# Optimization experiments

Measured on AMD Instinct MI355X. Metric: run time of the kernel, lower is better.

## Reference

```python
import jax, jax.numpy as jnp
import numpy as np

DIM_MSA = 256
DIM_PAIR = 128
DIM_HID = 32
EPS = 0.001
LN_EPS = 1e-5


def setup_inputs() -> dict:
    key = jax.random.key(0)
    ks = jax.random.split(key, 8)
    b, m, n = 1, 256, 384
    x = jax.random.normal(ks[0], (b, m, n, DIM_MSA), dtype=jnp.float32)
    mask = jax.random.randint(ks[1], (b, m, n), 0, 2).astype(jnp.int32)
    ln_g = jnp.ones((DIM_MSA,), jnp.float32)
    ln_b = jnp.zeros((DIM_MSA,), jnp.float32)
    s = 1.0 / np.sqrt(DIM_MSA)
    wl = jax.random.normal(ks[2], (DIM_MSA, DIM_HID), jnp.float32) * s
    bl = jnp.zeros((DIM_HID,), jnp.float32)
    wr = jax.random.normal(ks[3], (DIM_MSA, DIM_HID), jnp.float32) * s
    br = jnp.zeros((DIM_HID,), jnp.float32)
    wo = jax.random.normal(ks[4], (DIM_HID * DIM_HID, DIM_PAIR), jnp.float32) / np.sqrt(DIM_HID * DIM_HID)
    bo = jnp.zeros((DIM_PAIR,), jnp.float32)
    return {"x": x, "mask": mask, "ln_g": ln_g, "ln_b": ln_b,
            "wl": wl, "bl": bl, "wr": wr, "br": br, "wo": wo, "bo": bo}


def reference(x, mask, ln_g, ln_b, wl, bl, wr, br, wo, bo):
    # LayerNorm over last dim
    mu = jnp.mean(x, axis=-1, keepdims=True)
    var = jnp.mean(jnp.square(x - mu), axis=-1, keepdims=True)
    xn = (x - mu) * jax.lax.rsqrt(var + LN_EPS) * ln_g + ln_b
    left = xn @ wl + bl    # [b,m,n,c]
    right = xn @ wr + br   # [b,m,n,d]
    m = mask.astype(x.dtype)  # 0/1 mask [b,m,n]
    left = left * m[..., None]
    right = right * m[..., None]
    # masked outer-product sum over MSA dim m, no 6D materialization
    outer = jnp.einsum('bmic,bmjd->bijcd', left, right)
    b_, i_, j_ = outer.shape[0], outer.shape[1], outer.shape[2]
    outer = outer.reshape(b_, i_, j_, DIM_HID * DIM_HID)
    out = outer @ wo + bo  # [b,i,j,pairwise]
    cnt = jnp.einsum('bmi,bmj->bij', m, m)  # valid-pair counts
    return out / (cnt[..., None] + EPS)
```

## Files before the change

kernel.cpp:

```cpp
#include <hip/hip_runtime.h>
#include <hip/hip_bf16.h>
#include <stdint.h>


typedef float f32x4 __attribute__((ext_vector_type(4)));
typedef __bf16 bf16x8 __attribute__((ext_vector_type(8)));

#define NSEQ 384
#define NMSA 256

typedef const __attribute__((address_space(1))) unsigned int* gptr_t;
typedef __attribute__((address_space(3))) unsigned int* lptr_t;

__device__ __forceinline__ void gload_lds16(const void* g, void* l) {
    __builtin_amdgcn_global_load_lds((gptr_t)g, (lptr_t)l, 16, 0, 0);
}

__global__ __launch_bounds__(256) void prep_all_kernel(
    const float* __restrict__ wo,
    const float* __restrict__ wl, const float* __restrict__ wr,
    const float* __restrict__ bl, const float* __restrict__ br,
    const float* __restrict__ ln_g, const float* __restrict__ ln_b,
    const int* __restrict__ mask,
    __bf16* __restrict__ woT, __bf16* __restrict__ wg,
    float* __restrict__ Gc, float* __restrict__ B2,
    float* __restrict__ inv_cnt)
{
    const int blk = blockIdx.x;
    __shared__ int mi[NMSA];
    __shared__ float sg[4], sb[4];

    if (blk < 512) {
        int gid = blk * 256 + threadIdx.x;
        int p = gid >> 10, k = gid & 1023;
        woT[gid] = (__bf16)wo[k * 128 + p];
    } else if (blk < 576) {
        const int c = blk - 512;
        const int k = threadIdx.x;
        float w = (c < 32) ? wl[k * 32 + c] : wr[k * 32 + (c - 32)];
        __bf16 wgb = (__bf16)(w * ln_g[k]);
        wg[c * 256 + k] = wgb;
        float gsum = (float)wgb;
        float bsum = w * ln_b[k];
        for (int off = 32; off; off >>= 1) {
            gsum += __shfl_down(gsum, off);
            bsum += __shfl_down(bsum, off);
        }
        int wid = k >> 6, lane = k & 63;
        if (lane == 0) { sg[wid] = gsum; sb[wid] = bsum; }
        __syncthreads();
        if (k == 0) {
            Gc[c] = sg[0] + sg[1] + sg[2] + sg[3];
            B2[c] = sb[0] + sb[1] + sb[2] + sb[3] + ((c < 32) ? bl[c] : br[c - 32]);
        }
    } else {
        const int i = blk - 576;
        const int t = threadIdx.x;
        mi[t] = mask[t * NSEQ + i];
        __syncthreads();
        for (int j = t; j < NSEQ; j += 256) {
            int acc = 0;
            for (int m = 0; m < NMSA; ++m)
                acc += mi[m] & mask[m * NSEQ + j];
            inv_cnt[i * NSEQ + j] = 1.0f / ((float)acc + 0.001f);
        }
    }
}

__global__ __launch_bounds__(256) void ln_proj_kernel(
    const float* __restrict__ x, const int* __restrict__ mask,
    const __bf16* __restrict__ wg, const float* __restrict__ Gc,
    const float* __restrict__ B2,
    __bf16* __restrict__ leftT, __bf16* __restrict__ rightT)
{
    const int n = blockIdx.x % NSEQ;
    const int mh = blockIdx.x / NSEQ;
    const int m0 = mh * 128;
    const int tid = threadIdx.x;
    __shared__ __bf16 xnT[128 * 40];
    __shared__ float muS[128], rsS[128], maskS[128], GcS[64], B2S[64];

    if (tid < 64) { GcS[tid] = Gc[tid]; B2S[tid] = B2[tid]; }
    if (tid < 128) maskS[tid] = (float)mask[(m0 + tid) * NSEQ + n];

    const int wid = tid >> 6, lane = tid & 63;
    const int lhi = lane >> 4, llo = lane & 15;
    const int wrq = wid >> 1, wcq = wid & 1;
    float ps[4] = {}, pq[4] = {};
    f32x4 acc[2][4] = {};

    for (int k0 = 0; k0 < 256; k0 += 32) {
        #pragma unroll
        for (int cc = 0; cc < 4; ++cc) {
            int ch = tid + cc * 256;
            int mR = ch >> 3, c4 = ch & 7;
            f32x4 v = *reinterpret_cast<const f32x4*>(x + ((size_t)(m0 + mR) * NSEQ + n) * 256 + k0 + c4 * 4);
            ps[cc] += v[0] + v[1] + v[2] + v[3];
            pq[cc] += v[0]*v[0] + v[1]*v[1] + v[2]*v[2] + v[3]*v[3];
            __bf16* dst = xnT + mR * 40 + c4 * 4;
            dst[0] = (__bf16)v[0]; dst[1] = (__bf16)v[1];
            dst[2] = (__bf16)v[2]; dst[3] = (__bf16)v[3];
        }
        __syncthreads();
        bf16x8 af[2], bfr[4];
        #pragma unroll
        for (int fr = 0; fr < 2; ++fr)
            af[fr] = *reinterpret_cast<const bf16x8*>(wg + (size_t)(wrq * 32 + fr * 16 + llo) * 256 + k0 + lhi * 8);
        #pragma unroll
        for (int fc = 0; fc < 4; ++fc)
            bfr[fc] = *reinterpret_cast<const bf16x8*>(xnT + (wcq * 64 + fc * 16 + llo) * 40 + lhi * 8);
        #pragma unroll
        for (int fr = 0; fr < 2; ++fr)
            #pragma unroll
            for (int fc = 0; fc < 4; ++fc)
                acc[fr][fc] = __builtin_amdgcn_mfma_f32_16x16x32_bf16(af[fr], bfr[fc], acc[fr][fc], 0, 0, 0);
        __syncthreads();
    }

    #pragma unroll
    for (int cc = 0; cc < 4; ++cc) {
        float s = ps[cc], q = pq[cc];
        s += __shfl_xor(s, 1); q += __shfl_xor(q, 1);
        s += __shfl_xor(s, 2); q += __shfl_xor(q, 2);
        s += __shfl_xor(s, 4); q += __shfl_xor(q, 4);
        if ((tid & 7) == 0) {
            int mR = (tid >> 3) + cc * 32;
            float mu = s * (1.f / 256.f);
            float var = q * (1.f / 256.f) - mu * mu;
            muS[mR] = mu;
            rsS[mR] = rsqrtf(var + 1e-5f);
        }
    }
    __syncthreads();

    #pragma unroll
    for (int fr = 0; fr < 2; ++fr) {
        #pragma unroll
        for (int fc = 0; fc < 4; ++fc) {
            int mR = wcq * 64 + fc * 16 + llo;
            float mv = maskS[mR], rs = rsS[mR], mu = muS[mR];
            #pragma unroll
            for (int r = 0; r < 4; ++r) {
                int c = wrq * 32 + fr * 16 + lhi * 4 + r;
                float val = (acc[fr][fc][r] - mu * GcS[c]) * rs + B2S[c];
                __bf16 bv = (__bf16)(val * mv);
                if (c < 32) leftT [(size_t)(n * 32 + c)        * 256 + m0 + mR] = bv;
                else        rightT[(size_t)(n * 32 + (c - 32)) * 256 + m0 + mR] = bv;
            }
        }
    }
}

__global__ __launch_bounds__(512, 2) void outer_gemm_kernel(
    const __bf16* __restrict__ leftT, const __bf16* __restrict__ rightT,
    const __bf16* __restrict__ woT, const float* __restrict__ bo,
    const float* __restrict__ inv_cnt, float* __restrict__ out)
{
    __shared__ char smem[131072];
    const int tid = threadIdx.x;
    const int wid = tid >> 6, lane = tid & 63;
    const int lhi = lane >> 4, llo = lane & 15;
    const int wr = wid >> 2, wc = wid & 3;

    int wg_ = blockIdx.x;
    int l  = (wg_ & 7) * 288 + (wg_ >> 3);
    int bj = l / 48, bi = l % 48;

    char* Abuf[2] = { smem,         smem + 65536 };
    char* Bbuf[2] = { smem + 32768, smem + 98304 };

    auto STAGE = [&](int buf, int k0) {
        #pragma unroll
        for (int it = 0; it < 4; ++it) {
            int q = it * 512 + wid * 64 + lane;
            int r = q >> 3;
            int s = (q & 7) ^ (r & 7);
            int ldsoff = (it * 512 + wid * 64) * 16;
            gload_lds16(leftT  + (size_t)(bi * 256 + r) * 256 + k0 + s * 8, Abuf[buf] + ldsoff);
            gload_lds16(rightT + (size_t)(bj * 256 + r) * 256 + k0 + s * 8, Bbuf[buf] + ldsoff);
        }
    };

    f32x4 acc[8][4] = {};

    STAGE(0, 0);
    #pragma unroll
    for (int t = 0; t < 4; ++t) {
        if (t < 3) {
            STAGE((t + 1) & 1, (t + 1) * 64);
            asm volatile("s_waitcnt vmcnt(8)" ::: "memory");
        } else {
            asm volatile("s_waitcnt vmcnt(0)" ::: "memory");
        }
        __builtin_amdgcn_s_barrier();
        const __bf16* Al = (const __bf16*)Abuf[t & 1];
        const __bf16* Bl = (const __bf16*)Bbuf[t & 1];
        #pragma unroll
        for (int kk = 0; kk < 2; ++kk) {
            bf16x8 af[8], bfv[4];
            int sb = kk * 4 + lhi;
            #pragma unroll
            for (int fr = 0; fr < 8; ++fr) {
                int row = wr * 128 + fr * 16 + llo;
                af[fr] = *(const bf16x8*)(Al + row * 64 + ((sb ^ (row & 7)) << 3));
            }
            #pragma unroll
            for (int fc = 0; fc < 4; ++fc) {
                int row = wc * 64 + fc * 16 + llo;
                bfv[fc] = *(const bf16x8*)(Bl + row * 64 + ((sb ^ (row & 7)) << 3));
            }
            asm volatile("s_waitcnt lgkmcnt(0)" ::: "memory");
            __builtin_amdgcn_sched_barrier(0);
            __builtin_amdgcn_s_setprio(1);
            #pragma unroll
            for (int fr = 0; fr < 8; ++fr)
                #pragma unroll
                for (int fc = 0; fc < 4; ++fc)
                    acc[fr][fc] = __builtin_amdgcn_mfma_f32_16x16x32_bf16(af[fr], bfv[fc], acc[fr][fc], 0, 0, 0);
            __builtin_amdgcn_s_setprio(0);
            __builtin_amdgcn_s_barrier();
        }
    }

    __bf16* Aep = (__bf16*)smem;
    #pragma unroll
    for (int fr = 0; fr < 8; ++fr) {
        #pragma unroll
        for (int fc = 0; fc < 4; ++fc) {
            int gj = wc * 64 + fc * 16 + llo;
            int jl = gj >> 5, d = gj & 31;
            #pragma unroll
            for (int r = 0; r < 4; ++r) {
                int gi = wr * 128 + fr * 16 + lhi * 4 + r;
                int il = gi >> 5, c = gi & 31;
                int ij = il * 8 + jl;
                int cd = c * 32 + d;
                int s = cd >> 3;
                int ss = s ^ ((s >> 4) & 7) ^ (ij & 7);
                Aep[ij * 1024 + (ss << 3) + (cd & 7)] = (__bf16)acc[fr][fc][r];
            }
        }
    }
    __syncthreads();

    f32x4 eacc[4] = {};
    const int p = wid * 16 + llo;
    const __bf16* wrow = woT + (size_t)p * 1024 + lhi * 8;
    #pragma unroll 4
    for (int k0 = 0; k0 < 1024; k0 += 32) {
        int sb = (k0 >> 3) + lhi;
        bf16x8 bw = *(const bf16x8*)(wrow + k0);
        #pragma unroll
        for (int mf = 0; mf < 4; ++mf) {
            int ij = mf * 16 + llo;
            int ss = sb ^ ((sb >> 4) & 7) ^ (ij & 7);
            bf16x8 a = *(const bf16x8*)(Aep + ij * 1024 + (ss << 3));
            eacc[mf] = __builtin_amdgcn_mfma_f32_16x16x32_bf16(a, bw, eacc[mf], 0, 0, 0);
        }
    }

    const float bov = bo[p];
    #pragma unroll
    for (int mf = 0; mf < 4; ++mf) {
        #pragma unroll
        for (int r = 0; r < 4; ++r) {
            int ij = mf * 16 + lhi * 4 + r;
            int i = bi * 8 + (ij >> 3);
            int j = bj * 8 + (ij & 7);
            size_t idx = (size_t)i * NSEQ + j;
            out[idx * 128 + p] = (eacc[mf][r] + bov) * inv_cnt[idx];
        }
    }
}

extern "C" void kernel_launch(void* const* d_in, const int* in_sizes, int n_in,
                              void* d_out, int out_size, void* d_ws, size_t ws_size,
                              hipStream_t stream) {
    const float* x    = (const float*)d_in[0];
    const int*   mask = (const int*)  d_in[1];
    const float* ln_g = (const float*)d_in[2];
    const float* ln_b = (const float*)d_in[3];
    const float* wl   = (const float*)d_in[4];
    const float* bl   = (const float*)d_in[5];
    const float* wr   = (const float*)d_in[6];
    const float* br   = (const float*)d_in[7];
    const float* wo   = (const float*)d_in[8];
    const float* bo   = (const float*)d_in[9];
    float* out = (float*)d_out;

    char* ws = (char*)d_ws;
    __bf16* leftT   = (__bf16*)(ws);
    __bf16* rightT  = (__bf16*)(ws + 6291456);
    __bf16* woT     = (__bf16*)(ws + 12582912);
    __bf16* wg      = (__bf16*)(ws + 12845056);
    float*  Gc      = (float*) (ws + 12877824);
    float*  B2      = (float*) (ws + 12878080);
    float*  inv_cnt = (float*) (ws + 12878336);

    prep_all_kernel<<<960, 256, 0, stream>>>(wo, wl, wr, bl, br, ln_g, ln_b, mask,
                                             woT, wg, Gc, B2, inv_cnt);
    ln_proj_kernel<<<768, 256, 0, stream>>>(x, mask, wg, Gc, B2, leftT, rightT);
    outer_gemm_kernel<<<2304, 512, 0, stream>>>(leftT, rightT, woT, bo, inv_cnt, out);
}
```

Measured before the change: 204.2 us.

## Use 1024-thread workgroups with smaller per-wave tiles and vectorized epilogue stores

The outer-product GEMM now runs 16 waves per workgroup instead of 8. Each wave computes a 64x64 tile instead of 128x64, which halves the accumulator registers and the per-thread staging loads. The wo transpose is reordered to a d-major (d,c) K layout so each lane can write its four MFMA results to LDS as one bf16x4 store instead of four scalar stores. The explicit lgkmcnt wait and the per-kk barrier are dropped, and the second GEMM's rows are split across the two wave halves. This adds latency-hiding waves, but the launch bound of 1024 threads with minimum 4 blocks per CU is very tight on registers and may force spills, and each wave now reuses its loaded fragments across less work.

```diff
diff --git a/kernel.cpp b/kernel.cpp
--- a/kernel.cpp
+++ b/kernel.cpp
@@ -5,6 +5,7 @@
 
 typedef float f32x4 __attribute__((ext_vector_type(4)));
 typedef __bf16 bf16x8 __attribute__((ext_vector_type(8)));
+typedef __bf16 bf16x4 __attribute__((ext_vector_type(4)));
 
 #define NSEQ 384
 #define NMSA 256
@@ -32,8 +33,9 @@
 
     if (blk < 512) {
         int gid = blk * 256 + threadIdx.x;
-        int p = gid >> 10, k = gid & 1023;
-        woT[gid] = (__bf16)wo[k * 128 + p];
+        int p = gid >> 10, q = gid & 1023;
+        int d = q >> 5, c = q & 31;
+        woT[gid] = (__bf16)wo[(c * 32 + d) * 128 + p];
     } else if (blk < 576) {
         const int c = blk - 512;
         const int k = threadIdx.x;
@@ -151,7 +153,7 @@
     }
 }
 
-__global__ __launch_bounds__(512, 2) void outer_gemm_kernel(
+__global__ __launch_bounds__(1024, 4) void outer_gemm_kernel(
     const __bf16* __restrict__ leftT, const __bf16* __restrict__ rightT,
     const __bf16* __restrict__ woT, const float* __restrict__ bo,
     const float* __restrict__ inv_cnt, float* __restrict__ out)
@@ -171,24 +173,24 @@
 
     auto STAGE = [&](int buf, int k0) {
         #pragma unroll
-        for (int it = 0; it < 4; ++it) {
-            int q = it * 512 + wid * 64 + lane;
+        for (int it = 0; it < 2; ++it) {
+            int q = it * 1024 + wid * 64 + lane;
             int r = q >> 3;
             int s = (q & 7) ^ (r & 7);
-            int ldsoff = (it * 512 + wid * 64) * 16;
+            int ldsoff = (it * 1024 + wid * 64) * 16;
             gload_lds16(leftT  + (size_t)(bi * 256 + r) * 256 + k0 + s * 8, Abuf[buf] + ldsoff);
             gload_lds16(rightT + (size_t)(bj * 256 + r) * 256 + k0 + s * 8, Bbuf[buf] + ldsoff);
         }
     };
 
-    f32x4 acc[8][4] = {};
+    f32x4 acc[4][4] = {};
 
     STAGE(0, 0);
     #pragma unroll
     for (int t = 0; t < 4; ++t) {
         if (t < 3) {
             STAGE((t + 1) & 1, (t + 1) * 64);
-            asm volatile("s_waitcnt vmcnt(8)" ::: "memory");
+            asm volatile("s_waitcnt vmcnt(4)" ::: "memory");
         } else {
             asm volatile("s_waitcnt vmcnt(0)" ::: "memory");
         }
@@ -197,11 +199,11 @@
         const __bf16* Bl = (const __bf16*)Bbuf[t & 1];
         #pragma unroll
         for (int kk = 0; kk < 2; ++kk) {
-            bf16x8 af[8], bfv[4];
+            bf16x8 af[4], bfv[4];
             int sb = kk * 4 + lhi;
             #pragma unroll
-            for (int fr = 0; fr < 8; ++fr) {
-                int row = wr * 128 + fr * 16 + llo;
+            for (int fr = 0; fr < 4; ++fr) {
+                int row = wr * 64 + fr * 16 + llo;
                 af[fr] = *(const bf16x8*)(Al + row * 64 + ((sb ^ (row & 7)) << 3));
             }
             #pragma unroll
@@ -209,62 +211,56 @@
                 int row = wc * 64 + fc * 16 + llo;
                 bfv[fc] = *(const bf16x8*)(Bl + row * 64 + ((sb ^ (row & 7)) << 3));
             }
-            asm volatile("s_waitcnt lgkmcnt(0)" ::: "memory");
-            __builtin_amdgcn_sched_barrier(0);
             __builtin_amdgcn_s_setprio(1);
             #pragma unroll
-            for (int fr = 0; fr < 8; ++fr)
+            for (int fr = 0; fr < 4; ++fr)
                 #pragma unroll
                 for (int fc = 0; fc < 4; ++fc)
                     acc[fr][fc] = __builtin_amdgcn_mfma_f32_16x16x32_bf16(af[fr], bfv[fc], acc[fr][fc], 0, 0, 0);
             __builtin_amdgcn_s_setprio(0);
-            __builtin_amdgcn_s_barrier();
-        }
+        }
+        __builtin_amdgcn_s_barrier();
     }
 
     __bf16* Aep = (__bf16*)smem;
     #pragma unroll
-    for (int fr = 0; fr < 8; ++fr) {
+    for (int fr = 0; fr < 4; ++fr) {
         #pragma unroll
         for (int fc = 0; fc < 4; ++fc) {
-            int gj = wc * 64 + fc * 16 + llo;
-            int jl = gj >> 5, d = gj & 31;
-            #pragma unroll
-            for (int r = 0; r < 4; ++r) {
-                int gi = wr * 128 + fr * 16 + lhi * 4 + r;
-                int il = gi >> 5, c = gi & 31;
-                int ij = il * 8 + jl;
-                int cd = c * 32 + d;
-                int s = cd >> 3;
-                int ss = s ^ ((s >> 4) & 7) ^ (ij & 7);
-                Aep[ij * 1024 + (ss << 3) + (cd & 7)] = (__bf16)acc[fr][fc][r];
-            }
+            int ij = (wr * 2 + (fr >> 1)) * 8 + wc * 2 + (fc >> 1);
+            int tt = ((fc & 1) * 16 + llo) * 4 + (fr & 1) * 2 + (lhi >> 1);
+            int tp = tt ^ ((tt >> 4) & 7) ^ (ij & 7);
+            bf16x4 v;
+            v[0] = (__bf16)acc[fr][fc][0]; v[1] = (__bf16)acc[fr][fc][1];
+            v[2] = (__bf16)acc[fr][fc][2]; v[3] = (__bf16)acc[fr][fc][3];
+            *(bf16x4*)(Aep + ij * 1024 + tp * 8 + (lhi & 1) * 4) = v;
         }
     }
     __syncthreads();
 
-    f32x4 eacc[4] = {};
-    const int p = wid * 16 + llo;
+    f32x4 eacc[2] = {};
+    const int p = (wid & 7) * 16 + llo;
+    const int ijb = (wid >> 3) * 32;
     const __bf16* wrow = woT + (size_t)p * 1024 + lhi * 8;
     #pragma unroll 4
     for (int k0 = 0; k0 < 1024; k0 += 32) {
-        int sb = (k0 >> 3) + lhi;
+        int tb = (k0 >> 3) + lhi;
         bf16x8 bw = *(const bf16x8*)(wrow + k0);
         #pragma unroll
-        for (int mf = 0; mf < 4; ++mf) {
-            int ij = mf * 16 + llo;
-            int ss = sb ^ ((sb >> 4) & 7) ^ (ij & 7);
-            bf16x8 a = *(const bf16x8*)(Aep + ij * 1024 + (ss << 3));
+        for (int mf = 0; mf < 2; ++mf) {
+            int ij = ijb + mf * 16 + llo;
+            int tp = tb ^ ((tb >> 4) & 7) ^ (ij & 7);
+            bf16x8 a = *(const bf16x8*)(Aep + ij * 1024 + tp * 8);
             eacc[mf] = __builtin_amdgcn_mfma_f32_16x16x32_bf16(a, bw, eacc[mf], 0, 0, 0);
         }
     }
 
     const float bov = bo[p];
     #pragma unroll
-    for (int mf = 0; mf < 4; ++mf) {
+    for (int mf = 0; mf < 2; ++mf) {
         #pragma unroll
         for (int r = 0; r < 4; ++r) {
-            int ij = mf * 16 + lhi * 4 + r;
+            int ij = ijb + mf * 16 + lhi * 4 + r;
             int i = bi * 8 + (ij >> 3);
             int j = bj * 8 + (ij & 7);
             size_t idx = (size_t)i * NSEQ + j;
@@ -300,5 +296,5 @@
     prep_all_kernel<<<960, 256, 0, stream>>>(wo, wl, wr, bl, br, ln_g, ln_b, mask,
                                              woT, wg, Gc, B2, inv_cnt);
     ln_proj_kernel<<<768, 256, 0, stream>>>(x, mask, wg, Gc, B2, leftT, rightT);
-    outer_gemm_kernel<<<2304, 512, 0, stream>>>(leftT, rightT, woT, bo, inv_cnt, out);
-}
+    outer_gemm_kernel<<<2304, 1024, 0, stream>>>(leftT, rightT, woT, bo, inv_cnt, out);
+}
```

Result: slower. 257.9 us (+26.3%).

## Permute woT k-order to vectorize epilogue LDS stores and retile projection

Applied to the files above, without the earlier changes.

The woT prep now orders the K dimension as d-major/c-minor, so each MFMA accumulator's four consecutive rows can be written to LDS as one packed bf16x4 store with a new XOR swizzle, replacing scalar bf16 stores. The output projection is retiled so each wave handles 32 ij rows by 32 output channels (2x2 MFMA tiles), reusing each A fragment across two weight fragments and halving LDS reads of A per MFMA. The main loop also drops the per-kk waitcnt/sched_barrier/setprio and barrier, keeping a single wait and barrier after both kk steps. This trades explicit scheduling control for fewer synchronizations. The swizzle must stay consistent between the epilogue writes and reads.

```diff
diff --git a/kernel.cpp b/kernel.cpp
--- a/kernel.cpp
+++ b/kernel.cpp
@@ -5,6 +5,7 @@
 
 typedef float f32x4 __attribute__((ext_vector_type(4)));
 typedef __bf16 bf16x8 __attribute__((ext_vector_type(8)));
+typedef __bf16 bf16x4 __attribute__((ext_vector_type(4)));
 
 #define NSEQ 384
 #define NMSA 256
@@ -32,8 +33,9 @@
 
     if (blk < 512) {
         int gid = blk * 256 + threadIdx.x;
-        int p = gid >> 10, k = gid & 1023;
-        woT[gid] = (__bf16)wo[k * 128 + p];
+        int p = gid >> 10, q = gid & 1023;
+        int d = q >> 5, c = q & 31;
+        woT[gid] = (__bf16)wo[(c * 32 + d) * 128 + p];
     } else if (blk < 576) {
         const int c = blk - 512;
         const int k = threadIdx.x;
@@ -209,17 +211,14 @@
                 int row = wc * 64 + fc * 16 + llo;
                 bfv[fc] = *(const bf16x8*)(Bl + row * 64 + ((sb ^ (row & 7)) << 3));
             }
-            asm volatile("s_waitcnt lgkmcnt(0)" ::: "memory");
-            __builtin_amdgcn_sched_barrier(0);
-            __builtin_amdgcn_s_setprio(1);
             #pragma unroll
             for (int fr = 0; fr < 8; ++fr)
                 #pragma unroll
                 for (int fc = 0; fc < 4; ++fc)
                     acc[fr][fc] = __builtin_amdgcn_mfma_f32_16x16x32_bf16(af[fr], bfv[fc], acc[fr][fc], 0, 0, 0);
-            __builtin_amdgcn_s_setprio(0);
-            __builtin_amdgcn_s_barrier();
-        }
+        }
+        asm volatile("s_waitcnt lgkmcnt(0)" ::: "memory");
+        __builtin_amdgcn_s_barrier();
     }
 
     __bf16* Aep = (__bf16*)smem;
@@ -227,48 +226,51 @@
     for (int fr = 0; fr < 8; ++fr) {
         #pragma unroll
         for (int fc = 0; fc < 4; ++fc) {
-            int gj = wc * 64 + fc * 16 + llo;
-            int jl = gj >> 5, d = gj & 31;
-            #pragma unroll
-            for (int r = 0; r < 4; ++r) {
-                int gi = wr * 128 + fr * 16 + lhi * 4 + r;
-                int il = gi >> 5, c = gi & 31;
-                int ij = il * 8 + jl;
-                int cd = c * 32 + d;
-                int s = cd >> 3;
-                int ss = s ^ ((s >> 4) & 7) ^ (ij & 7);
-                Aep[ij * 1024 + (ss << 3) + (cd & 7)] = (__bf16)acc[fr][fc][r];
-            }
+            int ij = (wr * 4 + (fr >> 1)) * 8 + wc * 2 + (fc >> 1);
+            int t = ((fc & 1) * 16 + llo) * 4 + (fr & 1) * 2 + (lhi >> 1);
+            int phys = (((t & 3) << 5) | (t >> 2)) ^ (ij & 15);
+            bf16x4 v;
+            v[0] = (__bf16)acc[fr][fc][0]; v[1] = (__bf16)acc[fr][fc][1];
+            v[2] = (__bf16)acc[fr][fc][2]; v[3] = (__bf16)acc[fr][fc][3];
+            *(bf16x4*)(Aep + ij * 1024 + (phys << 3) + (lhi & 1) * 4) = v;
         }
     }
     __syncthreads();
 
-    f32x4 eacc[4] = {};
-    const int p = wid * 16 + llo;
-    const __bf16* wrow = woT + (size_t)p * 1024 + lhi * 8;
+    const int ih = wid >> 2, pg = wid & 3;
+    const int p0 = pg * 32;
+    f32x4 eacc[2][2] = {};
+    const __bf16* wrow0 = woT + (size_t)(p0 + llo)      * 1024 + lhi * 8;
+    const __bf16* wrow1 = woT + (size_t)(p0 + 16 + llo) * 1024 + lhi * 8;
     #pragma unroll 4
     for (int k0 = 0; k0 < 1024; k0 += 32) {
-        int sb = (k0 >> 3) + lhi;
-        bf16x8 bw = *(const bf16x8*)(wrow + k0);
-        #pragma unroll
-        for (int mf = 0; mf < 4; ++mf) {
-            int ij = mf * 16 + llo;
-            int ss = sb ^ ((sb >> 4) & 7) ^ (ij & 7);
-            bf16x8 a = *(const bf16x8*)(Aep + ij * 1024 + (ss << 3));
-            eacc[mf] = __builtin_amdgcn_mfma_f32_16x16x32_bf16(a, bw, eacc[mf], 0, 0, 0);
-        }
-    }
-
-    const float bov = bo[p];
-    #pragma unroll
-    for (int mf = 0; mf < 4; ++mf) {
-        #pragma unroll
-        for (int r = 0; r < 4; ++r) {
-            int ij = mf * 16 + lhi * 4 + r;
-            int i = bi * 8 + (ij >> 3);
-            int j = bj * 8 + (ij & 7);
-            size_t idx = (size_t)i * NSEQ + j;
-            out[idx * 128 + p] = (eacc[mf][r] + bov) * inv_cnt[idx];
+        bf16x8 bw0 = *(const bf16x8*)(wrow0 + k0);
+        bf16x8 bw1 = *(const bf16x8*)(wrow1 + k0);
+        int base = (lhi << 5) | (k0 >> 5);
+        #pragma unroll
+        for (int mf = 0; mf < 2; ++mf) {
+            int ij = ih * 32 + mf * 16 + llo;
+            int phys = base ^ llo;
+            bf16x8 a = *(const bf16x8*)(Aep + ij * 1024 + (phys << 3));
+            eacc[mf][0] = __builtin_amdgcn_mfma_f32_16x16x32_bf16(a, bw0, eacc[mf][0], 0, 0, 0);
+            eacc[mf][1] = __builtin_amdgcn_mfma_f32_16x16x32_bf16(a, bw1, eacc[mf][1], 0, 0, 0);
+        }
+    }
+
+    #pragma unroll
+    for (int pf = 0; pf < 2; ++pf) {
+        int p = p0 + pf * 16 + llo;
+        float bov = bo[p];
+        #pragma unroll
+        for (int mf = 0; mf < 2; ++mf) {
+            #pragma unroll
+            for (int r = 0; r < 4; ++r) {
+                int ij = ih * 32 + mf * 16 + lhi * 4 + r;
+                int i = bi * 8 + (ij >> 3);
+                int j = bj * 8 + (ij & 7);
+                size_t idx = (size_t)i * NSEQ + j;
+                out[idx * 128 + p] = (eacc[mf][pf][r] + bov) * inv_cnt[idx];
+            }
         }
     }
 }
```

Measured after the change: 251.2 us. 1.23x slower.
